# Performance work log

Hardware: AMD Instinct MI355X
Metric: run time of the kernel (lower is better)

## Reference

```python
import jax, jax.numpy as jnp
import numpy as np

N, E = 50000, 800000
IN_D, HID_D, OUT_D = 128, 64, 64
EPS_BN = 1e-5
NEG_SLOPE = 0.2


def _xavier(key, shape):
    fan_in, fan_out = shape[0], shape[-1]
    lim = float(np.sqrt(6.0 / (fan_in + fan_out)))
    return jax.random.uniform(key, shape, jnp.float32, -lim, lim)


def setup_inputs() -> dict:
    key = jax.random.key(0)
    ks = jax.random.split(key, 10)
    x = jax.random.normal(ks[0], (N, IN_D), jnp.float32)
    edge_index = jax.random.randint(ks[1], (2, E), 0, N, jnp.int64)
    return {
        "x": x,
        "edge_index": edge_index,
        "W1": _xavier(ks[2], (IN_D, HID_D)),
        "att_src1": _xavier(ks[3], (1, HID_D))[0],
        "att_dst1": _xavier(ks[4], (1, HID_D))[0],
        "bias1": jnp.zeros((HID_D,), jnp.float32),
        "gamma": jnp.ones((HID_D,), jnp.float32),
        "beta": jnp.zeros((HID_D,), jnp.float32),
        "W2": _xavier(ks[5], (HID_D, OUT_D)),
        "att_src2": _xavier(ks[6], (1, OUT_D))[0],
        "att_dst2": _xavier(ks[7], (1, OUT_D))[0],
        "bias2": jnp.zeros((OUT_D,), jnp.float32),
    }


def _gat_conv(x, src, dst, W, a_src, a_dst, bias, n_nodes):
    # h: [N, D_out]; messages flow src -> dst; softmax over edges per dst node
    h = x @ W
    alpha_s = h @ a_src  # [N]
    alpha_d = h @ a_dst  # [N]
    e = jax.nn.leaky_relu(alpha_s[src] + alpha_d[dst], NEG_SLOPE)  # [E]
    e_max = jax.ops.segment_max(e, dst, num_segments=n_nodes)
    e = jnp.exp(e - e_max[dst])
    denom = jax.ops.segment_sum(e, dst, num_segments=n_nodes)
    alpha = e / (denom[dst] + 1e-16)  # [E]
    out = jax.ops.segment_sum(h[src] * alpha[:, None], dst, num_segments=n_nodes)
    return out + bias


def _batchnorm(x, gamma, beta):
    mu = jnp.mean(x, axis=0)
    var = jnp.var(x, axis=0)
    return (x - mu) * jax.lax.rsqrt(var + EPS_BN) * gamma + beta


def reference(x, edge_index, W1, att_src1, att_dst1, bias1, gamma, beta,
              W2, att_src2, att_dst2, bias2):
    n_nodes = x.shape[0]
    loops = jnp.arange(n_nodes, dtype=edge_index.dtype)
    src = jnp.concatenate([edge_index[0], loops])  # add self loops (PyG default)
    dst = jnp.concatenate([edge_index[1], loops])
    h = _gat_conv(x, src, dst, W1, att_src1, att_dst1, bias1, n_nodes)
    h = jax.nn.relu(_batchnorm(h, gamma, beta))
    return _gat_conv(h, src, dst, W2, att_src2, att_dst2, bias2, n_nodes)
```

## Files before the change

kernel.cpp:

```cpp
#include <hip/hip_runtime.h>

#define N_NODES 50000
#define E_EDGES 800000
#define NE_TOT  (E_EDGES + N_NODES)
#define IND     128
#define HID     64
#define CAP_X   32
#define NEG_SLOPE 0.2f
#define GEMM_BLKS ((N_NODES + 63) / 64)
#define EDGE_BLKS ((NE_TOT + 255) / 256)

typedef short v8s __attribute__((ext_vector_type(8)));
typedef float v4f __attribute__((ext_vector_type(4)));

#define SWZ(row, byte) ((byte) ^ (((row) & 7) << 4))

static __device__ __forceinline__ unsigned short f2bf(float f) {
    unsigned u = __float_as_uint(f);
    return (unsigned short)((u + 0x7FFF + ((u >> 16) & 1)) >> 16);
}
static __device__ __forceinline__ float bf2f(unsigned short u) {
    return __uint_as_float(((unsigned)u) << 16);
}

__global__ void k_init(const float* __restrict__ W1, const float* __restrict__ W2,
                       int* __restrict__ cnt, float* __restrict__ sums,
                       unsigned short* __restrict__ w1t, unsigned short* __restrict__ w2t) {
    int g = blockIdx.x * 256 + threadIdx.x;
    if (g < 8 * N_NODES) cnt[g] = 0;
    if (g < 128) sums[g] = 0.f;
    if (g < 64 * IND) { int c = g >> 7, k = g & 127; w1t[g] = f2bf(W1[k * 64 + c]); }
    if (g < 64 * 64)  { int c = g >> 6, k = g & 63;  w2t[g] = f2bf(W2[k * 64 + c]); }
}

__global__ __launch_bounds__(256) void k_fused1(
    const float* __restrict__ x, const unsigned short* __restrict__ w1t,
    const float* __restrict__ as_w, const float* __restrict__ ad_w,
    unsigned short* __restrict__ hbf, float* __restrict__ as_out, float* __restrict__ ad_out,
    const int* __restrict__ ei, int* __restrict__ cnt, unsigned short* __restrict__ bucket)
{
    __shared__ __align__(16) char sA[64 * 256];
    __shared__ __align__(16) char sB[64 * 256];
    __shared__ float sAs[64], sAd[64];
    int tid = threadIdx.x;

    if (blockIdx.x >= GEMM_BLKS) {
        int xcc;
        asm("s_getreg_b32 %0, hwreg(20, 0, 32)" : "=s"(xcc));
        xcc &= 7;
        int e = (blockIdx.x - GEMM_BLKS) * 256 + tid;
        if (e >= NE_TOT) return;
        int s, d;
        if (e < E_EDGES) { s = ei[e]; d = ei[E_EDGES + e]; }
        else { s = d = e - E_EDGES; }
        int pos = atomicAdd(&cnt[xcc * N_NODES + d], 1);
        if (pos < CAP_X) bucket[((size_t)(xcc * CAP_X + pos)) * N_NODES + d] = (unsigned short)s;
        return;
    }

    int row0 = blockIdx.x * 64;
#pragma unroll
    for (int i = 0; i < 8; ++i) {
        int idx = i * 256 + tid;
        int r = idx >> 5, c4 = idx & 31;
        int gr = row0 + r; if (gr >= N_NODES) gr = N_NODES - 1;
        float4 v = ((const float4*)(x + (size_t)gr * IND))[c4];
        ushort4 b; b.x = f2bf(v.x); b.y = f2bf(v.y); b.z = f2bf(v.z); b.w = f2bf(v.w);
        *(ushort4*)(sA + r * 256 + SWZ(r, c4 * 8)) = b;
    }
#pragma unroll
    for (int i = 0; i < 4; ++i) {
        int idx = i * 256 + tid;
        int r = idx >> 4, c8 = idx & 15;
        v8s wv = *(const v8s*)(w1t + idx * 8);
        *(v8s*)(sB + r * 256 + SWZ(r, c8 * 16)) = wv;
    }
    if (tid < 64) { sAs[tid] = as_w[tid]; sAd[tid] = ad_w[tid]; }
    __syncthreads();

    int w = tid >> 6, lane = tid & 63;
    int arow = w * 16 + (lane & 15);
    int kb   = (lane >> 4) * 16;
    v4f acc[4] = {};
#pragma unroll
    for (int ks = 0; ks < 4; ++ks) {
        v8s a = *(const v8s*)(sA + arow * 256 + SWZ(arow, ks * 64 + kb));
#pragma unroll
        for (int ct = 0; ct < 4; ++ct) {
            int brow = ct * 16 + (lane & 15);
            v8s b = *(const v8s*)(sB + brow * 256 + SWZ(brow, ks * 64 + kb));
            acc[ct] = __builtin_amdgcn_mfma_f32_16x16x32_bf16(a, b, acc[ct], 0, 0, 0);
        }
    }

    int cbase = lane & 15;
    int rloc  = (lane >> 4) * 4;
#pragma unroll
    for (int rg = 0; rg < 4; ++rg) {
        float vs = 0.f, vd = 0.f;
#pragma unroll
        for (int ct = 0; ct < 4; ++ct) {
            vs = fmaf(acc[ct][rg], sAs[ct * 16 + cbase], vs);
            vd = fmaf(acc[ct][rg], sAd[ct * 16 + cbase], vd);
        }
        vs += __shfl_xor(vs, 1, 64); vd += __shfl_xor(vd, 1, 64);
        vs += __shfl_xor(vs, 2, 64); vd += __shfl_xor(vd, 2, 64);
        vs += __shfl_xor(vs, 4, 64); vd += __shfl_xor(vd, 4, 64);
        vs += __shfl_xor(vs, 8, 64); vd += __shfl_xor(vd, 8, 64);
        int row = row0 + w * 16 + rloc + rg;
        if (cbase == 0 && row < N_NODES) { as_out[row] = vs; ad_out[row] = vd; }
    }
    __syncthreads();
    unsigned short* sC = (unsigned short*)sA;
#pragma unroll
    for (int ct = 0; ct < 4; ++ct)
#pragma unroll
        for (int rg = 0; rg < 4; ++rg)
            sC[(w * 16 + rloc + rg) * 64 + ct * 16 + cbase] = f2bf(acc[ct][rg]);
    __syncthreads();
    int validc = min(64, N_NODES - row0) * 8;
#pragma unroll
    for (int i = 0; i < 2; ++i) {
        int c = i * 256 + tid;
        if (c < validc)
            *(v8s*)(hbf + (size_t)row0 * 64 + c * 8) = *(const v8s*)(sC + c * 8);
    }
}

template <bool OUT_BF16>
__global__ __launch_bounds__(256) void k_agg(
    const unsigned short* __restrict__ hin, const float* __restrict__ as_, const float* __restrict__ ad_,
    const int* __restrict__ cnt, const unsigned short* __restrict__ bucket,
    const float* __restrict__ bias, void* __restrict__ outv)
{
    int wave = threadIdx.x >> 6, lane = threadIdx.x & 63;
    int n0 = blockIdx.x * 8 + wave * 2;

    int deg[2], xseg[2], base[2], s_l[2];
    float e_[2], m_[2], w_l[2], denom[2];

#pragma unroll
    for (int j = 0; j < 2; ++j) {
        int n = n0 + j;
        int p[9]; p[0] = 0;
#pragma unroll
        for (int xx = 0; xx < 8; ++xx)
            p[xx + 1] = p[xx] + min(cnt[xx * N_NODES + n], CAP_X);
        deg[j] = min(p[8], 64);
        int xs = 0, bs = 0;
#pragma unroll
        for (int i = 0; i < 7; ++i)
            if (lane >= p[i + 1]) { xs = i + 1; bs = p[i + 1]; }
        xseg[j] = xs; base[j] = bs;
    }
#pragma unroll
    for (int j = 0; j < 2; ++j) {
        s_l[j] = 0; e_[j] = -1e30f;
        if (lane < deg[j]) {
            s_l[j] = (int)bucket[((size_t)(xseg[j] * CAP_X + (lane - base[j]))) * N_NODES + n0 + j];
            float t = as_[s_l[j]] + ad_[n0 + j];
            e_[j] = t > 0.f ? t : NEG_SLOPE * t;
        }
        m_[j] = e_[j];
    }
    for (int off = 32; off; off >>= 1) {
        m_[0] = fmaxf(m_[0], __shfl_xor(m_[0], off, 64));
        m_[1] = fmaxf(m_[1], __shfl_xor(m_[1], off, 64));
    }
#pragma unroll
    for (int j = 0; j < 2; ++j) {
        w_l[j] = (lane < deg[j]) ? __expf(e_[j] - m_[j]) : 0.f;
        denom[j] = w_l[j];
    }
    for (int off = 32; off; off >>= 1) {
        denom[0] += __shfl_xor(denom[0], off, 64);
        denom[1] += __shfl_xor(denom[1], off, 64);
    }

    int g = lane >> 4, fb = (lane & 15) * 4;
    float a[2][4] = {};
    int dmax = max(deg[0], deg[1]);
    for (int t = 0; t < dmax; t += 8) {
#pragma unroll
        for (int j = 0; j < 2; ++j) {
            int sa = __shfl(s_l[j], t + g);
            int sb = __shfl(s_l[j], t + 4 + g);
            float wa = __shfl(w_l[j], t + g);
            float wb = __shfl(w_l[j], t + 4 + g);
            ushort4 ha = *(const ushort4*)(hin + (size_t)sa * HID + fb);
            ushort4 hb = *(const ushort4*)(hin + (size_t)sb * HID + fb);
            a[j][0] = fmaf(wa, bf2f(ha.x), a[j][0]); a[j][1] = fmaf(wa, bf2f(ha.y), a[j][1]);
            a[j][2] = fmaf(wa, bf2f(ha.z), a[j][2]); a[j][3] = fmaf(wa, bf2f(ha.w), a[j][3]);
            a[j][0] = fmaf(wb, bf2f(hb.x), a[j][0]); a[j][1] = fmaf(wb, bf2f(hb.y), a[j][1]);
            a[j][2] = fmaf(wb, bf2f(hb.z), a[j][2]); a[j][3] = fmaf(wb, bf2f(hb.w), a[j][3]);
        }
    }
#pragma unroll
    for (int j = 0; j < 2; ++j)
#pragma unroll
        for (int k = 0; k < 4; ++k) {
            a[j][k] += __shfl_xor(a[j][k], 16, 64);
            a[j][k] += __shfl_xor(a[j][k], 32, 64);
        }

    if (lane < 16) {
        float4 b4 = ((const float4*)bias)[lane];
#pragma unroll
        for (int j = 0; j < 2; ++j) {
            float inv = 1.f / (denom[j] + 1e-16f);
            float r0 = fmaf(a[j][0], inv, b4.x), r1 = fmaf(a[j][1], inv, b4.y);
            float r2 = fmaf(a[j][2], inv, b4.z), r3 = fmaf(a[j][3], inv, b4.w);
            if (OUT_BF16) {
                ushort4 o; o.x = f2bf(r0); o.y = f2bf(r1); o.z = f2bf(r2); o.w = f2bf(r3);
                *(ushort4*)((unsigned short*)outv + (size_t)(n0 + j) * HID + lane * 4) = o;
            } else {
                float4 o = {r0, r1, r2, r3};
                *(float4*)((float*)outv + (size_t)(n0 + j) * HID + lane * 4) = o;
            }
        }
    }
}

__global__ __launch_bounds__(256) void k_bnstats(const unsigned short* __restrict__ h,
                                                 float* __restrict__ sums) {
    int lane = threadIdx.x & 63, wave = threadIdx.x >> 6;
    float s = 0.f, ss = 0.f;
    for (int r = blockIdx.x * 4 + wave; r < N_NODES; r += gridDim.x * 4) {
        float v = bf2f(h[(size_t)r * HID + lane]);
        s += v; ss = fmaf(v, v, ss);
    }
    __shared__ float ls[4][64], lss[4][64];
    ls[wave][lane] = s; lss[wave][lane] = ss;
    __syncthreads();
    if (wave == 0) {
        s  = ls[0][lane] + ls[1][lane] + ls[2][lane] + ls[3][lane];
        ss = lss[0][lane] + lss[1][lane] + lss[2][lane] + lss[3][lane];
        atomicAdd(&sums[lane], s);
        atomicAdd(&sums[64 + lane], ss);
    }
}

__global__ __launch_bounds__(256) void k_gemm2(
    const unsigned short* __restrict__ hin, const unsigned short* __restrict__ w2t,
    const float* __restrict__ sums, const float* __restrict__ gamma, const float* __restrict__ beta,
    const float* __restrict__ as_w, const float* __restrict__ ad_w,
    unsigned short* __restrict__ h2bf, float* __restrict__ as_out, float* __restrict__ ad_out)
{
    __shared__ __align__(16) char sA[64 * 128];
    __shared__ __align__(16) char sB[64 * 128];
    __shared__ float sAs[64], sAd[64], sScale[64], sShift[64];
    int tid = threadIdx.x;
    int row0 = blockIdx.x * 64;

    if (tid < 64) {
        float mean = sums[tid] * (1.f / N_NODES);
        float var  = sums[64 + tid] * (1.f / N_NODES) - mean * mean;
        float sc = gamma[tid] * rsqrtf(var + 1e-5f);
        sScale[tid] = sc;
        sShift[tid] = beta[tid] - mean * sc;
        sAs[tid] = as_w[tid]; sAd[tid] = ad_w[tid];
    }
    __syncthreads();

#pragma unroll
    for (int i = 0; i < 2; ++i) {
        int idx = i * 256 + tid;
        int r = idx >> 3, c8 = idx & 7;
        int gr = row0 + r; if (gr >= N_NODES) gr = N_NODES - 1;
        v8s hv = *(const v8s*)(hin + (size_t)gr * 64 + c8 * 8);
        unsigned short o[8];
#pragma unroll
        for (int j = 0; j < 8; ++j) {
            float f = bf2f((unsigned short)hv[j]);
            o[j] = f2bf(fmaxf(fmaf(f, sScale[c8 * 8 + j], sShift[c8 * 8 + j]), 0.f));
        }
        *(v8s*)(sA + r * 128 + SWZ(r, c8 * 16)) = *(v8s*)o;
    }
#pragma unroll
    for (int i = 0; i < 2; ++i) {
        int idx = i * 256 + tid;
        int r = idx >> 3, c8 = idx & 7;
        v8s wv = *(const v8s*)(w2t + idx * 8);
        *(v8s*)(sB + r * 128 + SWZ(r, c8 * 16)) = wv;
    }
    __syncthreads();

    int w = tid >> 6, lane = tid & 63;
    int arow = w * 16 + (lane & 15);
    int kb   = (lane >> 4) * 16;
    v4f acc[4] = {};
#pragma unroll
    for (int ks = 0; ks < 2; ++ks) {
        v8s a = *(const v8s*)(sA + arow * 128 + SWZ(arow, ks * 64 + kb));
#pragma unroll
        for (int ct = 0; ct < 4; ++ct) {
            int brow = ct * 16 + (lane & 15);
            v8s b = *(const v8s*)(sB + brow * 128 + SWZ(brow, ks * 64 + kb));
            acc[ct] = __builtin_amdgcn_mfma_f32_16x16x32_bf16(a, b, acc[ct], 0, 0, 0);
        }
    }

    int cbase = lane & 15;
    int rloc  = (lane >> 4) * 4;
#pragma unroll
    for (int rg = 0; rg < 4; ++rg) {
        float vs = 0.f, vd = 0.f;
#pragma unroll
        for (int ct = 0; ct < 4; ++ct) {
            vs = fmaf(acc[ct][rg], sAs[ct * 16 + cbase], vs);
            vd = fmaf(acc[ct][rg], sAd[ct * 16 + cbase], vd);
        }
        vs += __shfl_xor(vs, 1, 64); vd += __shfl_xor(vd, 1, 64);
        vs += __shfl_xor(vs, 2, 64); vd += __shfl_xor(vd, 2, 64);
        vs += __shfl_xor(vs, 4, 64); vd += __shfl_xor(vd, 4, 64);
        vs += __shfl_xor(vs, 8, 64); vd += __shfl_xor(vd, 8, 64);
        int row = row0 + w * 16 + rloc + rg;
        if (cbase == 0 && row < N_NODES) { as_out[row] = vs; ad_out[row] = vd; }
    }
    __syncthreads();
    unsigned short* sC = (unsigned short*)sA;
#pragma unroll
    for (int ct = 0; ct < 4; ++ct)
#pragma unroll
        for (int rg = 0; rg < 4; ++rg)
            sC[(w * 16 + rloc + rg) * 64 + ct * 16 + cbase] = f2bf(acc[ct][rg]);
    __syncthreads();
    int validc = min(64, N_NODES - row0) * 8;
#pragma unroll
    for (int i = 0; i < 2; ++i) {
        int c = i * 256 + tid;
        if (c < validc)
            *(v8s*)(h2bf + (size_t)row0 * 64 + c * 8) = *(const v8s*)(sC + c * 8);
    }
}

extern "C" void kernel_launch(void* const* d_in, const int* in_sizes, int n_in,
                              void* d_out, int out_size, void* d_ws, size_t ws_size,
                              hipStream_t stream) {
    const float* x        = (const float*)d_in[0];
    const int*   ei       = (const int*)d_in[1];
    const float* W1       = (const float*)d_in[2];
    const float* att_src1 = (const float*)d_in[3];
    const float* att_dst1 = (const float*)d_in[4];
    const float* bias1    = (const float*)d_in[5];
    const float* gamma    = (const float*)d_in[6];
    const float* beta     = (const float*)d_in[7];
    const float* W2       = (const float*)d_in[8];
    const float* att_src2 = (const float*)d_in[9];
    const float* att_dst2 = (const float*)d_in[10];
    const float* bias2    = (const float*)d_in[11];
    float* out = (float*)d_out;

    char* ws = (char*)d_ws;
    size_t off = 0;
    auto alloc = [&](size_t bytes) { void* p = ws + off; off = (off + bytes + 255) & ~(size_t)255; return p; };
    unsigned short* h1     = (unsigned short*)alloc((size_t)N_NODES * HID * 2);
    float* as1    = (float*)alloc((size_t)N_NODES * 4);
    float* ad1    = (float*)alloc((size_t)N_NODES * 4);
    unsigned short* h1agg  = (unsigned short*)alloc((size_t)N_NODES * HID * 2);
    unsigned short* h2     = (unsigned short*)alloc((size_t)N_NODES * HID * 2);
    float* as2    = (float*)alloc((size_t)N_NODES * 4);
    float* ad2    = (float*)alloc((size_t)N_NODES * 4);
    int*   cnt    = (int*)alloc((size_t)8 * N_NODES * 4);
    unsigned short* bucket = (unsigned short*)alloc((size_t)8 * CAP_X * N_NODES * 2);
    float* sums   = (float*)alloc(128 * 4);
    unsigned short* w1t = (unsigned short*)alloc(64 * IND * 2);
    unsigned short* w2t = (unsigned short*)alloc(64 * 64 * 2);

    int initBlocks = (8 * N_NODES + 255) / 256;
    k_init<<<initBlocks, 256, 0, stream>>>(W1, W2, cnt, sums, w1t, w2t);
    k_fused1<<<GEMM_BLKS + EDGE_BLKS, 256, 0, stream>>>(x, w1t, att_src1, att_dst1,
                                                        h1, as1, ad1, ei, cnt, bucket);
    k_agg<true><<<N_NODES / 8, 256, 0, stream>>>(h1, as1, ad1, cnt, bucket, bias1, h1agg);
    k_bnstats<<<256, 256, 0, stream>>>(h1agg, sums);
    k_gemm2<<<GEMM_BLKS, 256, 0, stream>>>(h1agg, w2t, sums, gamma, beta,
                                           att_src2, att_dst2, h2, as2, ad2);
    k_agg<false><<<N_NODES / 8, 256, 0, stream>>>(h2, as2, ad2, cnt, bucket, bias2, out);
}
```

Measured before the change: 122.9 us.

## Fuse BN statistics into layer-1 aggregation and make aggregation a persistent grid

```diff
diff --git a/kernel.cpp b/kernel.cpp
--- a/kernel.cpp
+++ b/kernel.cpp
@@ -9,6 +9,7 @@
 #define NEG_SLOPE 0.2f
 #define GEMM_BLKS ((N_NODES + 63) / 64)
 #define EDGE_BLKS ((NE_TOT + 255) / 256)
+#define AGG_BLKS  256
 
 typedef short v8s __attribute__((ext_vector_type(8)));
 typedef float v4f __attribute__((ext_vector_type(4)));
@@ -116,127 +117,145 @@
     for (int ct = 0; ct < 4; ++ct)
 #pragma unroll
         for (int rg = 0; rg < 4; ++rg)
-            sC[(w * 16 + rloc + rg) * 64 + ct * 16 + cbase] = f2bf(acc[ct][rg]);
+            sC[(w * 16 + rloc + rg) * 72 + ct * 16 + cbase] = f2bf(acc[ct][rg]);
     __syncthreads();
     int validc = min(64, N_NODES - row0) * 8;
 #pragma unroll
     for (int i = 0; i < 2; ++i) {
         int c = i * 256 + tid;
         if (c < validc)
-            *(v8s*)(hbf + (size_t)row0 * 64 + c * 8) = *(const v8s*)(sC + c * 8);
-    }
-}
-
-template <bool OUT_BF16>
+            *(v8s*)(hbf + (size_t)row0 * 64 + c * 8) = *(const v8s*)(sC + (c >> 3) * 72 + (c & 7) * 8);
+    }
+}
+
+template <bool OUT_BF16, bool BN_ACC>
 __global__ __launch_bounds__(256) void k_agg(
     const unsigned short* __restrict__ hin, const float* __restrict__ as_, const float* __restrict__ ad_,
     const int* __restrict__ cnt, const unsigned short* __restrict__ bucket,
-    const float* __restrict__ bias, void* __restrict__ outv)
+    const float* __restrict__ bias, void* __restrict__ outv, float* __restrict__ sums)
 {
     int wave = threadIdx.x >> 6, lane = threadIdx.x & 63;
-    int n0 = blockIdx.x * 8 + wave * 2;
-
-    int deg[2], xseg[2], base[2], s_l[2];
-    float e_[2], m_[2], w_l[2], denom[2];
-
-#pragma unroll
-    for (int j = 0; j < 2; ++j) {
-        int n = n0 + j;
-        int p[9]; p[0] = 0;
-#pragma unroll
-        for (int xx = 0; xx < 8; ++xx)
-            p[xx + 1] = p[xx] + min(cnt[xx * N_NODES + n], CAP_X);
-        deg[j] = min(p[8], 64);
-        int xs = 0, bs = 0;
-#pragma unroll
-        for (int i = 0; i < 7; ++i)
-            if (lane >= p[i + 1]) { xs = i + 1; bs = p[i + 1]; }
-        xseg[j] = xs; base[j] = bs;
-    }
-#pragma unroll
-    for (int j = 0; j < 2; ++j) {
-        s_l[j] = 0; e_[j] = -1e30f;
-        if (lane < deg[j]) {
-            s_l[j] = (int)bucket[((size_t)(xseg[j] * CAP_X + (lane - base[j]))) * N_NODES + n0 + j];
-            float t = as_[s_l[j]] + ad_[n0 + j];
-            e_[j] = t > 0.f ? t : NEG_SLOPE * t;
-        }
-        m_[j] = e_[j];
-    }
-    for (int off = 32; off; off >>= 1) {
-        m_[0] = fmaxf(m_[0], __shfl_xor(m_[0], off, 64));
-        m_[1] = fmaxf(m_[1], __shfl_xor(m_[1], off, 64));
-    }
-#pragma unroll
-    for (int j = 0; j < 2; ++j) {
-        w_l[j] = (lane < deg[j]) ? __expf(e_[j] - m_[j]) : 0.f;
-        denom[j] = w_l[j];
-    }
-    for (int off = 32; off; off >>= 1) {
-        denom[0] += __shfl_xor(denom[0], off, 64);
-        denom[1] += __shfl_xor(denom[1], off, 64);
-    }
-
     int g = lane >> 4, fb = (lane & 15) * 4;
-    float a[2][4] = {};
-    int dmax = max(deg[0], deg[1]);
-    for (int t = 0; t < dmax; t += 8) {
-#pragma unroll
-        for (int j = 0; j < 2; ++j) {
-            int sa = __shfl(s_l[j], t + g);
-            int sb = __shfl(s_l[j], t + 4 + g);
-            float wa = __shfl(w_l[j], t + g);
-            float wb = __shfl(w_l[j], t + 4 + g);
-            ushort4 ha = *(const ushort4*)(hin + (size_t)sa * HID + fb);
-            ushort4 hb = *(const ushort4*)(hin + (size_t)sb * HID + fb);
-            a[j][0] = fmaf(wa, bf2f(ha.x), a[j][0]); a[j][1] = fmaf(wa, bf2f(ha.y), a[j][1]);
-            a[j][2] = fmaf(wa, bf2f(ha.z), a[j][2]); a[j][3] = fmaf(wa, bf2f(ha.w), a[j][3]);
-            a[j][0] = fmaf(wb, bf2f(hb.x), a[j][0]); a[j][1] = fmaf(wb, bf2f(hb.y), a[j][1]);
-            a[j][2] = fmaf(wb, bf2f(hb.z), a[j][2]); a[j][3] = fmaf(wb, bf2f(hb.w), a[j][3]);
-        }
-    }
-#pragma unroll
-    for (int j = 0; j < 2; ++j)
-#pragma unroll
-        for (int k = 0; k < 4; ++k) {
-            a[j][k] += __shfl_xor(a[j][k], 16, 64);
-            a[j][k] += __shfl_xor(a[j][k], 32, 64);
-        }
-
-    if (lane < 16) {
-        float4 b4 = ((const float4*)bias)[lane];
-#pragma unroll
-        for (int j = 0; j < 2; ++j) {
-            float inv = 1.f / (denom[j] + 1e-16f);
-            float r0 = fmaf(a[j][0], inv, b4.x), r1 = fmaf(a[j][1], inv, b4.y);
-            float r2 = fmaf(a[j][2], inv, b4.z), r3 = fmaf(a[j][3], inv, b4.w);
-            if (OUT_BF16) {
-                ushort4 o; o.x = f2bf(r0); o.y = f2bf(r1); o.z = f2bf(r2); o.w = f2bf(r3);
-                *(ushort4*)((unsigned short*)outv + (size_t)(n0 + j) * HID + lane * 4) = o;
-            } else {
-                float4 o = {r0, r1, r2, r3};
-                *(float4*)((float*)outv + (size_t)(n0 + j) * HID + lane * 4) = o;
-            }
-        }
-    }
-}
-
-__global__ __launch_bounds__(256) void k_bnstats(const unsigned short* __restrict__ h,
-                                                 float* __restrict__ sums) {
-    int lane = threadIdx.x & 63, wave = threadIdx.x >> 6;
-    float s = 0.f, ss = 0.f;
-    for (int r = blockIdx.x * 4 + wave; r < N_NODES; r += gridDim.x * 4) {
-        float v = bf2f(h[(size_t)r * HID + lane]);
-        s += v; ss = fmaf(v, v, ss);
-    }
-    __shared__ float ls[4][64], lss[4][64];
-    ls[wave][lane] = s; lss[wave][lane] = ss;
-    __syncthreads();
-    if (wave == 0) {
-        s  = ls[0][lane] + ls[1][lane] + ls[2][lane] + ls[3][lane];
-        ss = lss[0][lane] + lss[1][lane] + lss[2][lane] + lss[3][lane];
-        atomicAdd(&sums[lane], s);
-        atomicAdd(&sums[64 + lane], ss);
+    float4 b4 = ((const float4*)bias)[lane & 15];
+    float bnS[4] = {}, bnQ[4] = {};
+
+    const int NITER = (N_NODES + AGG_BLKS * 8 - 1) / (AGG_BLKS * 8);
+    for (int it = 0; it < NITER; ++it) {
+        int n0 = (it * AGG_BLKS + blockIdx.x) * 8 + wave * 2;
+        if (n0 < N_NODES) {
+            int deg[2], xseg[2], base[2], s_l[2];
+            float e_[2], m_[2], w_l[2], denom[2];
+#pragma unroll
+            for (int j = 0; j < 2; ++j) {
+                int n = n0 + j;
+                int p[9]; p[0] = 0;
+#pragma unroll
+                for (int xx = 0; xx < 8; ++xx)
+                    p[xx + 1] = p[xx] + min(cnt[xx * N_NODES + n], CAP_X);
+                deg[j] = min(p[8], 64);
+                int xs = 0, bs = 0;
+#pragma unroll
+                for (int i = 0; i < 7; ++i)
+                    if (lane >= p[i + 1]) { xs = i + 1; bs = p[i + 1]; }
+                xseg[j] = xs; base[j] = bs;
+            }
+#pragma unroll
+            for (int j = 0; j < 2; ++j) {
+                s_l[j] = 0; e_[j] = -1e30f;
+                if (lane < deg[j]) {
+                    s_l[j] = (int)bucket[((size_t)(xseg[j] * CAP_X + (lane - base[j]))) * N_NODES + n0 + j];
+                    float t = as_[s_l[j]] + ad_[n0 + j];
+                    e_[j] = t > 0.f ? t : NEG_SLOPE * t;
+                }
+                m_[j] = e_[j];
+            }
+            for (int off = 32; off; off >>= 1) {
+                m_[0] = fmaxf(m_[0], __shfl_xor(m_[0], off, 64));
+                m_[1] = fmaxf(m_[1], __shfl_xor(m_[1], off, 64));
+            }
+#pragma unroll
+            for (int j = 0; j < 2; ++j) {
+                w_l[j] = (lane < deg[j]) ? __expf(e_[j] - m_[j]) : 0.f;
+                denom[j] = w_l[j];
+            }
+            for (int off = 32; off; off >>= 1) {
+                denom[0] += __shfl_xor(denom[0], off, 64);
+                denom[1] += __shfl_xor(denom[1], off, 64);
+            }
+
+            float a[2][4] = {};
+            int dmax = max(deg[0], deg[1]);
+            for (int t = 0; t < dmax; t += 8) {
+#pragma unroll
+                for (int j = 0; j < 2; ++j) {
+                    int sa = __shfl(s_l[j], t + g);
+                    int sb = __shfl(s_l[j], t + 4 + g);
+                    float wa = __shfl(w_l[j], t + g);
+                    float wb = __shfl(w_l[j], t + 4 + g);
+                    ushort4 ha = *(const ushort4*)(hin + (size_t)sa * HID + fb);
+                    ushort4 hb = *(const ushort4*)(hin + (size_t)sb * HID + fb);
+                    a[j][0] = fmaf(wa, bf2f(ha.x), a[j][0]); a[j][1] = fmaf(wa, bf2f(ha.y), a[j][1]);
+                    a[j][2] = fmaf(wa, bf2f(ha.z), a[j][2]); a[j][3] = fmaf(wa, bf2f(ha.w), a[j][3]);
+                    a[j][0] = fmaf(wb, bf2f(hb.x), a[j][0]); a[j][1] = fmaf(wb, bf2f(hb.y), a[j][1]);
+                    a[j][2] = fmaf(wb, bf2f(hb.z), a[j][2]); a[j][3] = fmaf(wb, bf2f(hb.w), a[j][3]);
+                }
+            }
+#pragma unroll
+            for (int j = 0; j < 2; ++j)
+#pragma unroll
+                for (int k = 0; k < 4; ++k) {
+                    a[j][k] += __shfl_xor(a[j][k], 16, 64);
+                    a[j][k] += __shfl_xor(a[j][k], 32, 64);
+                }
+
+            if (lane < 16) {
+#pragma unroll
+                for (int j = 0; j < 2; ++j) {
+                    float inv = 1.f / (denom[j] + 1e-16f);
+                    float r[4];
+                    r[0] = fmaf(a[j][0], inv, b4.x); r[1] = fmaf(a[j][1], inv, b4.y);
+                    r[2] = fmaf(a[j][2], inv, b4.z); r[3] = fmaf(a[j][3], inv, b4.w);
+                    if (BN_ACC) {
+#pragma unroll
+                        for (int k = 0; k < 4; ++k) {
+                            float rb = bf2f(f2bf(r[k]));
+                            bnS[k] += rb; bnQ[k] = fmaf(rb, rb, bnQ[k]);
+                        }
+                    }
+                    if (OUT_BF16) {
+                        ushort4 o; o.x = f2bf(r[0]); o.y = f2bf(r[1]); o.z = f2bf(r[2]); o.w = f2bf(r[3]);
+                        *(ushort4*)((unsigned short*)outv + (size_t)(n0 + j) * HID + lane * 4) = o;
+                    } else {
+                        float4 o = {r[0], r[1], r[2], r[3]};
+                        *(float4*)((float*)outv + (size_t)(n0 + j) * HID + lane * 4) = o;
+                    }
+                }
+            }
+        }
+    }
+
+    if (BN_ACC) {
+        __shared__ float bnLDS[4][16][8];
+        if (lane < 16) {
+#pragma unroll
+            for (int k = 0; k < 4; ++k) {
+                bnLDS[wave][lane][k] = bnS[k];
+                bnLDS[wave][lane][4 + k] = bnQ[k];
+            }
+        }
+        __syncthreads();
+        int tid = threadIdx.x;
+        if (tid < 64) {
+            int f = tid;
+            float s = 0.f, q = 0.f;
+#pragma unroll
+            for (int w2 = 0; w2 < 4; ++w2) {
+                s += bnLDS[w2][f >> 2][f & 3];
+                q += bnLDS[w2][f >> 2][4 + (f & 3)];
+            }
+            atomicAdd(&sums[f], s);
+            atomicAdd(&sums[64 + f], q);
+        }
     }
 }
 
@@ -246,7 +265,7 @@
     const float* __restrict__ as_w, const float* __restrict__ ad_w,
     unsigned short* __restrict__ h2bf, float* __restrict__ as_out, float* __restrict__ ad_out)
 {
-    __shared__ __align__(16) char sA[64 * 128];
+    __shared__ __align__(16) char sA[64 * 160];
     __shared__ __align__(16) char sB[64 * 128];
     __shared__ float sAs[64], sAd[64], sScale[64], sShift[64];
     int tid = threadIdx.x;
@@ -323,14 +342,14 @@
     for (int ct = 0; ct < 4; ++ct)
 #pragma unroll
         for (int rg = 0; rg < 4; ++rg)
-            sC[(w * 16 + rloc + rg) * 64 + ct * 16 + cbase] = f2bf(acc[ct][rg]);
+            sC[(w * 16 + rloc + rg) * 72 + ct * 16 + cbase] = f2bf(acc[ct][rg]);
     __syncthreads();
     int validc = min(64, N_NODES - row0) * 8;
 #pragma unroll
     for (int i = 0; i < 2; ++i) {
         int c = i * 256 + tid;
         if (c < validc)
-            *(v8s*)(h2bf + (size_t)row0 * 64 + c * 8) = *(const v8s*)(sC + c * 8);
+            *(v8s*)(h2bf + (size_t)row0 * 64 + c * 8) = *(const v8s*)(sC + (c >> 3) * 72 + (c & 7) * 8);
     }
 }
 
@@ -371,9 +390,8 @@
     k_init<<<initBlocks, 256, 0, stream>>>(W1, W2, cnt, sums, w1t, w2t);
     k_fused1<<<GEMM_BLKS + EDGE_BLKS, 256, 0, stream>>>(x, w1t, att_src1, att_dst1,
                                                         h1, as1, ad1, ei, cnt, bucket);
-    k_agg<true><<<N_NODES / 8, 256, 0, stream>>>(h1, as1, ad1, cnt, bucket, bias1, h1agg);
-    k_bnstats<<<256, 256, 0, stream>>>(h1agg, sums);
+    k_agg<true, true><<<AGG_BLKS, 256, 0, stream>>>(h1, as1, ad1, cnt, bucket, bias1, h1agg, sums);
     k_gemm2<<<GEMM_BLKS, 256, 0, stream>>>(h1agg, w2t, sums, gamma, beta,
                                            att_src2, att_dst2, h2, as2, ad2);
-    k_agg<false><<<N_NODES / 8, 256, 0, stream>>>(h2, as2, ad2, cnt, bucket, bias2, out);
-}
+    k_agg<false, false><<<AGG_BLKS, 256, 0, stream>>>(h2, as2, ad2, cnt, bucket, bias2, out, nullptr);
+}
```

After: 235.5 us. +91.6%, slower.

## Compact bucketed adjacency into per-node rows and pad LDS epilogue stride

Applied to the files above, without the earlier changes.

```diff
diff --git a/kernel.cpp b/kernel.cpp
--- a/kernel.cpp
+++ b/kernel.cpp
@@ -116,49 +116,60 @@
     for (int ct = 0; ct < 4; ++ct)
 #pragma unroll
         for (int rg = 0; rg < 4; ++rg)
-            sC[(w * 16 + rloc + rg) * 64 + ct * 16 + cbase] = f2bf(acc[ct][rg]);
+            sC[(w * 16 + rloc + rg) * 72 + ct * 16 + cbase] = f2bf(acc[ct][rg]);
     __syncthreads();
     int validc = min(64, N_NODES - row0) * 8;
 #pragma unroll
     for (int i = 0; i < 2; ++i) {
         int c = i * 256 + tid;
         if (c < validc)
-            *(v8s*)(hbf + (size_t)row0 * 64 + c * 8) = *(const v8s*)(sC + c * 8);
-    }
+            *(v8s*)(hbf + (size_t)row0 * 64 + c * 8) = *(const v8s*)(sC + (c >> 3) * 72 + (c & 7) * 8);
+    }
+}
+
+__global__ __launch_bounds__(64) void k_compact(
+    const int* __restrict__ cnt, const unsigned short* __restrict__ bucket,
+    unsigned short* __restrict__ adjT, int* __restrict__ degT)
+{
+    int lane = threadIdx.x;
+    int n = blockIdx.x * 64 + lane;
+    bool ok = n < N_NODES;
+    unsigned short* row = adjT + (size_t)n * 64;
+    int deg = 0;
+#pragma unroll
+    for (int xcc = 0; xcc < 8; ++xcc) {
+        int cx = ok ? min(cnt[xcc * N_NODES + n], CAP_X) : 0;
+        int smax = cx;
+        for (int off = 32; off; off >>= 1) smax = max(smax, __shfl_xor(smax, off, 64));
+        for (int s = 0; s < smax; ++s) {
+            unsigned short v = 0;
+            if (ok) v = bucket[((size_t)(xcc * CAP_X + s)) * N_NODES + n];
+            if (s < cx && deg < 64) { row[deg] = v; ++deg; }
+        }
+    }
+    if (ok) degT[n] = deg;
 }
 
 template <bool OUT_BF16>
 __global__ __launch_bounds__(256) void k_agg(
     const unsigned short* __restrict__ hin, const float* __restrict__ as_, const float* __restrict__ ad_,
-    const int* __restrict__ cnt, const unsigned short* __restrict__ bucket,
+    const int* __restrict__ degT, const unsigned short* __restrict__ adjT,
     const float* __restrict__ bias, void* __restrict__ outv)
 {
     int wave = threadIdx.x >> 6, lane = threadIdx.x & 63;
     int n0 = blockIdx.x * 8 + wave * 2;
 
-    int deg[2], xseg[2], base[2], s_l[2];
+    int deg[2], s_l[2];
     float e_[2], m_[2], w_l[2], denom[2];
 
 #pragma unroll
     for (int j = 0; j < 2; ++j) {
         int n = n0 + j;
-        int p[9]; p[0] = 0;
-#pragma unroll
-        for (int xx = 0; xx < 8; ++xx)
-            p[xx + 1] = p[xx] + min(cnt[xx * N_NODES + n], CAP_X);
-        deg[j] = min(p[8], 64);
-        int xs = 0, bs = 0;
-#pragma unroll
-        for (int i = 0; i < 7; ++i)
-            if (lane >= p[i + 1]) { xs = i + 1; bs = p[i + 1]; }
-        xseg[j] = xs; base[j] = bs;
-    }
-#pragma unroll
-    for (int j = 0; j < 2; ++j) {
+        deg[j] = degT[n];
         s_l[j] = 0; e_[j] = -1e30f;
         if (lane < deg[j]) {
-            s_l[j] = (int)bucket[((size_t)(xseg[j] * CAP_X + (lane - base[j]))) * N_NODES + n0 + j];
-            float t = as_[s_l[j]] + ad_[n0 + j];
+            s_l[j] = (int)adjT[(size_t)n * 64 + lane];
+            float t = as_[s_l[j]] + ad_[n];
             e_[j] = t > 0.f ? t : NEG_SLOPE * t;
         }
         m_[j] = e_[j];
@@ -246,7 +257,7 @@
     const float* __restrict__ as_w, const float* __restrict__ ad_w,
     unsigned short* __restrict__ h2bf, float* __restrict__ as_out, float* __restrict__ ad_out)
 {
-    __shared__ __align__(16) char sA[64 * 128];
+    __shared__ __align__(16) char sA[64 * 160];
     __shared__ __align__(16) char sB[64 * 128];
     __shared__ float sAs[64], sAd[64], sScale[64], sShift[64];
     int tid = threadIdx.x;
@@ -323,14 +334,14 @@
     for (int ct = 0; ct < 4; ++ct)
 #pragma unroll
         for (int rg = 0; rg < 4; ++rg)
-            sC[(w * 16 + rloc + rg) * 64 + ct * 16 + cbase] = f2bf(acc[ct][rg]);
+            sC[(w * 16 + rloc + rg) * 72 + ct * 16 + cbase] = f2bf(acc[ct][rg]);
     __syncthreads();
     int validc = min(64, N_NODES - row0) * 8;
 #pragma unroll
     for (int i = 0; i < 2; ++i) {
         int c = i * 256 + tid;
         if (c < validc)
-            *(v8s*)(h2bf + (size_t)row0 * 64 + c * 8) = *(const v8s*)(sC + c * 8);
+            *(v8s*)(h2bf + (size_t)row0 * 64 + c * 8) = *(const v8s*)(sC + (c >> 3) * 72 + (c & 7) * 8);
     }
 }
 
@@ -363,17 +374,22 @@
     float* ad2    = (float*)alloc((size_t)N_NODES * 4);
     int*   cnt    = (int*)alloc((size_t)8 * N_NODES * 4);
     unsigned short* bucket = (unsigned short*)alloc((size_t)8 * CAP_X * N_NODES * 2);
+    unsigned short* adjT   = (unsigned short*)alloc((size_t)N_NODES * 64 * 2);
+    int*   degT   = (int*)alloc((size_t)N_NODES * 4);
     float* sums   = (float*)alloc(128 * 4);
     unsigned short* w1t = (unsigned short*)alloc(64 * IND * 2);
     unsigned short* w2t = (unsigned short*)alloc(64 * 64 * 2);
 
     int initBlocks = (8 * N_NODES + 255) / 256;
+    int aggBlocks  = (N_NODES + 7) / 8;
+    int cmpBlocks  = (N_NODES + 63) / 64;
     k_init<<<initBlocks, 256, 0, stream>>>(W1, W2, cnt, sums, w1t, w2t);
     k_fused1<<<GEMM_BLKS + EDGE_BLKS, 256, 0, stream>>>(x, w1t, att_src1, att_dst1,
                                                         h1, as1, ad1, ei, cnt, bucket);
-    k_agg<true><<<N_NODES / 8, 256, 0, stream>>>(h1, as1, ad1, cnt, bucket, bias1, h1agg);
+    k_compact<<<cmpBlocks, 64, 0, stream>>>(cnt, bucket, adjT, degT);
+    k_agg<true><<<aggBlocks, 256, 0, stream>>>(h1, as1, ad1, degT, adjT, bias1, h1agg);
     k_bnstats<<<256, 256, 0, stream>>>(h1agg, sums);
     k_gemm2<<<GEMM_BLKS, 256, 0, stream>>>(h1agg, w2t, sums, gamma, beta,
                                            att_src2, att_dst2, h2, as2, ad2);
-    k_agg<false><<<N_NODES / 8, 256, 0, stream>>>(h2, as2, ad2, cnt, bucket, bias2, out);
-}
+    k_agg<false><<<aggBlocks, 256, 0, stream>>>(h2, as2, ad2, degT, adjT, bias2, out);
+}
```

Measured after the change: 143.5 us. 16.8% more time.
